# Kernel optimization log

Measured on AMD Instinct MI355X. Metric: run time of the kernel, lower is better.

## Reference

```python
import jax, jax.numpy as jnp
import numpy as np

N = 50000   # nodes
E = 600000  # edges
D = 128     # in/out features


def setup_inputs() -> dict:
    key = jax.random.key(0)
    k1, k2, k3, k4, k5, k6 = jax.random.split(key, 6)
    input = jax.random.normal(k1, (N, D), dtype=jnp.float32)
    W = jax.random.normal(k2, (D, D), dtype=jnp.float32) * (1.0 / np.sqrt(D))
    b = jax.random.normal(k3, (D,), dtype=jnp.float32) * 0.01
    adj_row = jnp.sort(jax.random.randint(k4, (E,), 0, N, dtype=jnp.int32))
    adj_col = jax.random.randint(k5, (E,), 0, N, dtype=jnp.int32)
    adj_val = jax.random.uniform(k6, (E,), dtype=jnp.float32)
    return {"input": input, "W": W, "b": b,
            "adj_row": adj_row, "adj_col": adj_col, "adj_val": adj_val}


def reference(input, W, b, adj_row, adj_col, adj_val):
    # support = Linear(input)  -> [N, D]
    support = jnp.einsum('nd,od->no', input, W) + b
    # sparse adj (COO) @ support : gather source rows, scale by edge value,
    # scatter-add into destination rows.
    msgs = support[adj_col] * adj_val[:, None]           # [E, D]
    agg = jax.ops.segment_sum(msgs, adj_row, num_segments=input.shape[0])
    return jnp.tanh(agg)
```

## Files before the change

kernel.cpp:

```cpp
#include <hip/hip_runtime.h>
#include <hip/hip_fp16.h>
#include <cmath>

#define DF 128

typedef _Float16 f16x8 __attribute__((ext_vector_type(8)));
typedef float    f32x4 __attribute__((ext_vector_type(4)));

__global__ __launch_bounds__(256)
void gemm_mfma_kernel(const float* __restrict__ X, const _Float16* __restrict__ Wh,
                      const float* __restrict__ bias, __half* __restrict__ S,
                      int N)
{
    const int wave = threadIdx.x >> 6;
    const int lane = threadIdx.x & 63;
    const int l15  = lane & 15;
    const int q    = lane >> 4;
    const int m0   = (blockIdx.x * 4 + wave) * 16;
    if (m0 >= N) return;

    f32x4 acc[8];
    #pragma unroll
    for (int nt = 0; nt < 8; ++nt) acc[nt] = (f32x4){0.f, 0.f, 0.f, 0.f};

    const int arow = min(m0 + l15, N - 1);
    #pragma unroll
    for (int kc = 0; kc < DF; kc += 32) {
        const float* xp = X + (size_t)arow * DF + kc + q * 8;
        float4 xa = *(const float4*)xp;
        float4 xb = *(const float4*)(xp + 4);
        f16x8 A;
        A[0] = (_Float16)xa.x; A[1] = (_Float16)xa.y;
        A[2] = (_Float16)xa.z; A[3] = (_Float16)xa.w;
        A[4] = (_Float16)xb.x; A[5] = (_Float16)xb.y;
        A[6] = (_Float16)xb.z; A[7] = (_Float16)xb.w;
        #pragma unroll
        for (int nt = 0; nt < 8; ++nt) {
            f16x8 B = *(const f16x8*)(Wh + (size_t)(nt * 16 + l15) * DF + kc + q * 8);
            acc[nt] = __builtin_amdgcn_mfma_f32_16x16x32_f16(A, B, acc[nt], 0, 0, 0);
        }
    }

    #pragma unroll
    for (int nt = 0; nt < 8; ++nt) {
        float bj = bias[nt * 16 + l15];
        #pragma unroll
        for (int r = 0; r < 4; ++r) {
            int gr = m0 + q * 4 + r;
            if (gr < N)
                S[(size_t)gr * DF + nt * 16 + l15] = __float2half(acc[nt][r] + bj);
        }
    }
}

__global__ __launch_bounds__(256)
void build_meta_kernel(const int* __restrict__ arow, const int* __restrict__ acol,
                       const float* __restrict__ aval, const float* __restrict__ W,
                       int* __restrict__ rowptr, int2* __restrict__ pk,
                       _Float16* __restrict__ Wh, int N, int E)
{
    int e = blockIdx.x * 256 + threadIdx.x;
    if (e >= E) return;
    if (e < DF * DF) Wh[e] = (_Float16)W[e];
    pk[e] = make_int2(acol[e] << 8, __float_as_int(aval[e]));
    int r = arow[e];
    int rprev = (e == 0) ? -1 : arow[e - 1];
    for (int n = rprev + 1; n <= r; ++n) rowptr[n] = e;
    if (e == E - 1) {
        for (int n = r + 1; n <= N; ++n) rowptr[n] = E;
    }
}

__global__ __launch_bounds__(256)
void agg_tanh_kernel(const __half* __restrict__ S, const int* __restrict__ rowptr,
                     const int2* __restrict__ pk, float* __restrict__ out, int Nn)
{
    const int n = __builtin_amdgcn_readfirstlane(blockIdx.x * 4 + (threadIdx.x >> 6));
    if (n >= Nn) return;
    const int lane = threadIdx.x & 63;
    const int l4   = lane * 4;

    const int start = rowptr[n];
    const int end   = rowptr[n + 1];
    const char* Sb  = (const char*)S;

    float2 a0; a0.x = 0.f; a0.y = 0.f;
    float2 a1; a1.x = 0.f; a1.y = 0.f;

    int e = start;
    for (; e + 8 <= end; e += 8) {
        __half2 h[8]; float v[8];
        #pragma unroll
        for (int u = 0; u < 8; ++u) {
            int2 p = pk[e + u];
            h[u] = *(const __half2*)(Sb + (size_t)(unsigned)p.x + l4);
            v[u] = __int_as_float(p.y);
        }
        #pragma unroll
        for (int u = 0; u < 8; ++u) {
            float2 s = __half22float2(h[u]);
            if (u & 1) { a1.x += v[u] * s.x; a1.y += v[u] * s.y; }
            else       { a0.x += v[u] * s.x; a0.y += v[u] * s.y; }
        }
    }
    if (e + 4 <= end) {
        __half2 h[4]; float v[4];
        #pragma unroll
        for (int u = 0; u < 4; ++u) {
            int2 p = pk[e + u];
            h[u] = *(const __half2*)(Sb + (size_t)(unsigned)p.x + l4);
            v[u] = __int_as_float(p.y);
        }
        #pragma unroll
        for (int u = 0; u < 4; ++u) {
            float2 s = __half22float2(h[u]);
            if (u & 1) { a1.x += v[u] * s.x; a1.y += v[u] * s.y; }
            else       { a0.x += v[u] * s.x; a0.y += v[u] * s.y; }
        }
        e += 4;
    }
    for (; e < end; ++e) {
        int2 p = pk[e];
        float2 s = __half22float2(*(const __half2*)(Sb + (size_t)(unsigned)p.x + l4));
        float v = __int_as_float(p.y);
        a0.x += v * s.x; a0.y += v * s.y;
    }

    float2 o;
    o.x = tanhf(a0.x + a1.x);
    o.y = tanhf(a0.y + a1.y);
    *(float2*)(out + (size_t)n * DF + lane * 2) = o;
}

extern "C" void kernel_launch(void* const* d_in, const int* in_sizes, int n_in,
                              void* d_out, int out_size, void* d_ws, size_t ws_size,
                              hipStream_t stream)
{
    const float* X    = (const float*)d_in[0];
    const float* W    = (const float*)d_in[1];
    const float* bias = (const float*)d_in[2];
    const int*   arow = (const int*)  d_in[3];
    const int*   acol = (const int*)  d_in[4];
    const float* aval = (const float*)d_in[5];
    float* out = (float*)d_out;

    const int N = in_sizes[0] / DF;
    const int E = in_sizes[3];

    __half*   S      = (__half*)d_ws;
    _Float16* Wh     = (_Float16*)((char*)d_ws + (size_t)N * DF * sizeof(__half));
    int*      rowptr = (int*)((char*)Wh + (size_t)DF * DF * sizeof(_Float16));
    int2*     pk     = (int2*)(rowptr + (N + 2));

    build_meta_kernel<<<(E + 255) / 256, 256, 0, stream>>>(arow, acol, aval, W,
                                                           rowptr, pk, Wh, N, E);

    const int mstrips = (N + 15) / 16;
    gemm_mfma_kernel<<<(mstrips + 3) / 4, 256, 0, stream>>>(X, Wh, bias, S, N);

    agg_tanh_kernel<<<(N + 3) / 4, 256, 0, stream>>>(S, rowptr, pk, out, N);
}
```

Baseline: 131.8 us.

## Stage W in padded LDS for GEMM and use 16-byte gathers in aggregation

The GEMM kernel now copies the fp16 weight matrix into padded shared memory once per block and reads B fragments from LDS instead of global memory. The aggregation kernel is restructured so each wave handles 8 edges per iteration, with 16 lanes per edge each loading 8 halfs (16 bytes), then combines the partial sums across lane groups with shuffles before tanh. This targets memory-instruction count and latency in the gather, at the cost of idle lanes on short rows and an extra LDS fill per GEMM block.

```diff
diff --git a/kernel.cpp b/kernel.cpp
--- a/kernel.cpp
+++ b/kernel.cpp
@@ -3,6 +3,7 @@
 #include <cmath>
 
 #define DF 128
+#define WPITCHH 136
 
 typedef _Float16 f16x8 __attribute__((ext_vector_type(8)));
 typedef float    f32x4 __attribute__((ext_vector_type(4)));
@@ -12,11 +13,23 @@
                       const float* __restrict__ bias, __half* __restrict__ S,
                       int N)
 {
-    const int wave = threadIdx.x >> 6;
-    const int lane = threadIdx.x & 63;
+    __shared__ _Float16 Wl[DF * WPITCHH];
+
+    const int t    = threadIdx.x;
+    const int lane = t & 63;
     const int l15  = lane & 15;
     const int q    = lane >> 4;
-    const int m0   = (blockIdx.x * 4 + wave) * 16;
+    const int m0   = (blockIdx.x * 4 + (t >> 6)) * 16;
+
+    #pragma unroll
+    for (int l = 0; l < 8; ++l) {
+        int flat = l * 256 + t;
+        int r    = flat >> 4;
+        int c8   = (flat & 15) * 8;
+        f16x8 v = *(const f16x8*)(Wh + (size_t)r * DF + c8);
+        *(f16x8*)(Wl + r * WPITCHH + c8) = v;
+    }
+    __syncthreads();
     if (m0 >= N) return;
 
     f32x4 acc[8];
@@ -36,7 +49,7 @@
         A[6] = (_Float16)xb.z; A[7] = (_Float16)xb.w;
         #pragma unroll
         for (int nt = 0; nt < 8; ++nt) {
-            f16x8 B = *(const f16x8*)(Wh + (size_t)(nt * 16 + l15) * DF + kc + q * 8);
+            f16x8 B = *(const f16x8*)(Wl + (nt * 16 + l15) * WPITCHH + kc + q * 8);
             acc[nt] = __builtin_amdgcn_mfma_f32_16x16x32_f16(A, B, acc[nt], 0, 0, 0);
         }
     }
@@ -78,58 +91,47 @@
     const int n = __builtin_amdgcn_readfirstlane(blockIdx.x * 4 + (threadIdx.x >> 6));
     if (n >= Nn) return;
     const int lane = threadIdx.x & 63;
-    const int l4   = lane * 4;
+    const int g    = lane >> 4;
+    const int fb   = (lane & 15) * 16;
 
     const int start = rowptr[n];
     const int end   = rowptr[n + 1];
     const char* Sb  = (const char*)S;
 
-    float2 a0; a0.x = 0.f; a0.y = 0.f;
-    float2 a1; a1.x = 0.f; a1.y = 0.f;
+    float acc[8];
+    #pragma unroll
+    for (int i = 0; i < 8; ++i) acc[i] = 0.f;
 
-    int e = start;
-    for (; e + 8 <= end; e += 8) {
-        __half2 h[8]; float v[8];
+    for (int base = start; base < end; base += 8) {
+        const int e0 = base + g;
+        const int e1 = base + 4 + g;
+        int2 p0 = (e0 < end) ? pk[e0] : make_int2(0, 0);
+        int2 p1 = (e1 < end) ? pk[e1] : make_int2(0, 0);
+        f16x8 h0 = *(const f16x8*)(Sb + (size_t)(unsigned)p0.x + fb);
+        f16x8 h1 = *(const f16x8*)(Sb + (size_t)(unsigned)p1.x + fb);
+        const float v0 = __int_as_float(p0.y);
+        const float v1 = __int_as_float(p1.y);
         #pragma unroll
-        for (int u = 0; u < 8; ++u) {
-            int2 p = pk[e + u];
-            h[u] = *(const __half2*)(Sb + (size_t)(unsigned)p.x + l4);
-            v[u] = __int_as_float(p.y);
-        }
-        #pragma unroll
-        for (int u = 0; u < 8; ++u) {
-            float2 s = __half22float2(h[u]);
-            if (u & 1) { a1.x += v[u] * s.x; a1.y += v[u] * s.y; }
-            else       { a0.x += v[u] * s.x; a0.y += v[u] * s.y; }
-        }
-    }
-    if (e + 4 <= end) {
-        __half2 h[4]; float v[4];
-        #pragma unroll
-        for (int u = 0; u < 4; ++u) {
-            int2 p = pk[e + u];
-            h[u] = *(const __half2*)(Sb + (size_t)(unsigned)p.x + l4);
-            v[u] = __int_as_float(p.y);
-        }
-        #pragma unroll
-        for (int u = 0; u < 4; ++u) {
-            float2 s = __half22float2(h[u]);
-            if (u & 1) { a1.x += v[u] * s.x; a1.y += v[u] * s.y; }
-            else       { a0.x += v[u] * s.x; a0.y += v[u] * s.y; }
-        }
-        e += 4;
-    }
-    for (; e < end; ++e) {
-        int2 p = pk[e];
-        float2 s = __half22float2(*(const __half2*)(Sb + (size_t)(unsigned)p.x + l4));
-        float v = __int_as_float(p.y);
-        a0.x += v * s.x; a0.y += v * s.y;
+        for (int i = 0; i < 8; ++i)
+            acc[i] += (float)h0[i] * v0 + (float)h1[i] * v1;
     }
 
-    float2 o;
-    o.x = tanhf(a0.x + a1.x);
-    o.y = tanhf(a0.y + a1.y);
-    *(float2*)(out + (size_t)n * DF + lane * 2) = o;
+    #pragma unroll
+    for (int i = 0; i < 8; ++i) {
+        acc[i] += __shfl_xor(acc[i], 16);
+        acc[i] += __shfl_xor(acc[i], 32);
+    }
+
+    if (g == 0) {
+        float4 o0, o1;
+        o0.x = tanhf(acc[0]); o0.y = tanhf(acc[1]);
+        o0.z = tanhf(acc[2]); o0.w = tanhf(acc[3]);
+        o1.x = tanhf(acc[4]); o1.y = tanhf(acc[5]);
+        o1.z = tanhf(acc[6]); o1.w = tanhf(acc[7]);
+        float* op = out + (size_t)n * DF + (lane & 15) * 8;
+        *(float4*)op       = o0;
+        *(float4*)(op + 4) = o1;
+    }
 }
 
 extern "C" void kernel_launch(void* const* d_in, const int* in_sizes, int n_in,
@@ -155,8 +157,7 @@
     build_meta_kernel<<<(E + 255) / 256, 256, 0, stream>>>(arow, acol, aval, W,
                                                            rowptr, pk, Wh, N, E);
 
-    const int mstrips = (N + 15) / 16;
-    gemm_mfma_kernel<<<(mstrips + 3) / 4, 256, 0, stream>>>(X, Wh, bias, S, N);
+    gemm_mfma_kernel<<<(N + 63) / 64, 256, 0, stream>>>(X, Wh, bias, S, N);
 
     agg_tanh_kernel<<<(N + 3) / 4, 256, 0, stream>>>(S, rowptr, pk, out, N);
 }
```

After: 129.0 us. 2.1% less time.
